# Optimization experiments

Hardware: AMD Instinct MI355X
Metric: run time of the kernel (lower is better)

## Reference

```python
import jax, jax.numpy as jnp
import numpy as np

EPS = 1e-5  # torch InstanceNorm2d default eps


def _attend(x_q, x_kv, Wq, Wk, Wv, Wo):
    # x_q, x_kv: [B, N, C]
    B, N, _ = x_q.shape
    q = x_q @ Wq            # [B, N, CH]
    k = x_kv @ Wk           # [B, N, CH]
    v = x_kv @ Wv           # [B, N, CH]
    CH = q.shape[-1]
    # rearrange 'b n c -> n (b c)' : [N, B*CH]; the torch repeat across batch
    # is redundant (same K/V for every query sample), so we keep one copy.
    kcat = jnp.transpose(k, (1, 0, 2)).reshape(N, B * CH)
    vcat = jnp.transpose(v, (1, 0, 2)).reshape(N, B * CH)
    # scores[b, i, j] = sum_n q[b, n, i] * kcat[n, j]  -> [B, CH, B*CH]
    scores = jnp.einsum('bni,nj->bij', q, kcat)
    # InstanceNorm2d(1): per-sample normalization over the (CH, B*CH) plane
    mu = scores.mean(axis=(1, 2), keepdims=True)
    var = scores.var(axis=(1, 2), keepdims=True)  # biased var, matches torch
    scores = (scores - mu) * jax.lax.rsqrt(var + EPS)
    attn = jax.nn.softmax(scores, axis=-1)        # softmax over j (dim=3)
    # ctx[b, n, i] = sum_j attn[b, i, j] * vcat[n, j]  -> [B, N, CH]
    ctx = jnp.einsum('bij,nj->bni', attn, vcat)
    return ctx @ Wo  # [B, N, C]


def setup_inputs() -> dict:
    key = jax.random.key(0)
    k0, k1, k2, k3, k4 = jax.random.split(key, 5)
    C, H = 64, 8
    CH = C * H
    emb = jax.random.normal(k0, (16, 2048, C), dtype=jnp.float32)
    s = 0.02
    Wq = jax.random.normal(k1, (C, CH), dtype=jnp.float32) * s
    Wk = jax.random.normal(k2, (C, CH), dtype=jnp.float32) * s
    Wv = jax.random.normal(k3, (C, CH), dtype=jnp.float32) * s
    Wo = jax.random.normal(k4, (CH, C), dtype=jnp.float32) * s
    return {"emb": emb, "Wq": Wq, "Wk": Wk, "Wv": Wv, "Wo": Wo}


def reference(emb, Wq, Wk, Wv, Wo):
    emb_l, emb_u = jnp.split(emb, 2, axis=0)
    emb_u_sg = jax.lax.stop_gradient(emb_u)  # emb_u is detached in the torch code
    out_u2l = _attend(emb_u_sg, emb_l, Wq, Wk, Wv, Wo)
    out_l2u = _attend(emb_l, emb_u_sg, Wq, Wk, Wv, Wo)
    return jnp.concatenate([out_l2u, out_u2l], axis=0)
```

## Files before the change

kernel.cpp:

```cpp
#include <hip/hip_runtime.h>
#include <hip/hip_fp16.h>

#define EPS 1e-5f

typedef __attribute__((ext_vector_type(8))) _Float16 half8;
typedef __attribute__((ext_vector_type(4))) _Float16 half4;
typedef __attribute__((ext_vector_type(4))) float float4v;

__device__ __forceinline__ float rv_from(const float* sums2, int db)
{
    float s1 = 0.f, s2 = 0.f;
#pragma unroll
    for (int p = 0; p < 8; p++) {
        s1 += sums2[(db * 8 + p) * 2];
        s2 += sums2[(db * 8 + p) * 2 + 1];
    }
    const float inv = 1.f / 2097152.f;
    float mu = s1 * inv;
    float var = s2 * inv - mu * mu;
    return rsqrtf(var + EPS);
}

__global__ __launch_bounds__(256)
void convT_k(const float* __restrict__ emb, const float* __restrict__ Wq,
             const float* __restrict__ Wk, const float* __restrict__ Wv,
             const float* __restrict__ Wo, __half* __restrict__ emb16,
             __half* __restrict__ embT16, __half* __restrict__ WkT16,
             __half* __restrict__ Wo16, __half* __restrict__ Wv16,
             float* __restrict__ GWQpart, float* __restrict__ wsp,
             __half* __restrict__ WqT16h, __half* __restrict__ WqT16l)
{
    __shared__ __align__(16) char smem[18432];
    const int tid = threadIdx.x;
    const int bid = blockIdx.x;

    if (bid < 256) {
        __half (*T)[136] = (__half(*)[136])smem;
        const int bb = bid >> 4;
        const int t0 = (bid & 15) * 128;
        const float* src = emb + (long long)bb * 131072 + (long long)t0 * 64;
        __half* d16 = emb16 + (long long)bb * 131072 + (long long)t0 * 64;
#pragma unroll
        for (int it = 0; it < 8; it++) {
            int e = (tid + it * 256) * 4;
            int t = e >> 6, c = e & 63;
            float4 v = *(const float4*)(src + t * 64 + c);
            half4 h;
            h[0] = (_Float16)v.x; h[1] = (_Float16)v.y;
            h[2] = (_Float16)v.z; h[3] = (_Float16)v.w;
            *(half4*)(d16 + t * 64 + c) = h;
            T[c + 0][t] = (__half)h[0];
            T[c + 1][t] = (__half)h[1];
            T[c + 2][t] = (__half)h[2];
            T[c + 3][t] = (__half)h[3];
        }
        __syncthreads();
        __half* dT = embT16 + (long long)bb * 131072 + t0;
#pragma unroll
        for (int it = 0; it < 4; it++) {
            int e = (tid + it * 256) * 8;
            int c = e >> 7, tt = e & 127;
            *(half8*)(dT + (long long)c * 2048 + tt) = *(const half8*)&T[c][tt];
        }
    } else if (bid < 272) {
        float (*t)[65] = (float(*)[65])smem;
        const int which = (bid - 256) >> 3;
        const int c0 = ((bid - 256) & 7) * 64;
        const int c = tid & 63, r4 = tid >> 6;
        if (which == 0) {
#pragma unroll
            for (int rr = r4; rr < 64; rr += 4)
                t[rr][c] = Wk[rr * 512 + c0 + c];
            __syncthreads();
#pragma unroll
            for (int rr = r4; rr < 64; rr += 4)
                WkT16[(c0 + rr) * 64 + c] = __float2half(t[c][rr]);
        } else {
#pragma unroll
            for (int rr = r4; rr < 64; rr += 4)
                t[rr][c] = Wo[(c0 + rr) * 64 + c];
            __syncthreads();
#pragma unroll
            for (int rr = r4; rr < 64; rr += 4)
                Wo16[rr * 512 + c0 + c] = __float2half(t[c][rr]);
        }
    } else if (bid < 280) {
        const int base = (bid - 272) * 4096;
#pragma unroll
        for (int it = 0; it < 4; it++) {
            int e = base + (tid + it * 256) * 4;
            float4 v = *(const float4*)(Wv + e);
            *(__half2*)(Wv16 + e)     = __floats2half2_rn(v.x, v.y);
            *(__half2*)(Wv16 + e + 2) = __floats2half2_rn(v.z, v.w);
        }
    } else if (bid < 296) {
        float (*Wl)[68] = (float(*)[68])smem;
        const int t2 = bid - 280;
        const int which = t2 >> 3;
        const int sl = t2 & 7;
        const int i0 = sl * 64;
        const float* W = which ? Wq : Wk;
        float* Gout = GWQpart + (long long)(which * 8 + sl) * 4096;
#pragma unroll
        for (int it = 0; it < 4; it++) {
            int e = tid + it * 256;
            int cc = e >> 4, i4 = (e & 15) * 4;
            *(float4*)&Wl[cc][i4] = *(const float4*)(W + cc * 512 + i0 + i4);
        }
        __syncthreads();
        if (tid < 64) {
            float s = 0.f;
#pragma unroll
            for (int j = 0; j < 64; j++) s += Wl[tid][j];
            wsp[(which * 8 + sl) * 64 + tid] = s;
        }
        const int cr = tid >> 2, cg = (tid & 3) * 16;
        float p[16] = {};
        for (int k = 0; k < 64; k++) {
            float a = Wl[cr][k];
#pragma unroll
            for (int j = 0; j < 16; j++) p[j] += a * Wl[cg + j][k];
        }
#pragma unroll
        for (int j = 0; j < 16; j++)
            Gout[cr * 64 + cg + j] = p[j];
    } else {
        float (*t)[65] = (float(*)[65])smem;
        const int i0 = (bid - 296) * 64;
        const int c = tid & 63, r4 = tid >> 6;
#pragma unroll
        for (int rr = r4; rr < 64; rr += 4)
            t[rr][c] = Wq[rr * 512 + i0 + c];
        __syncthreads();
#pragma unroll
        for (int rr = r4; rr < 64; rr += 4) {
            float x = t[c][rr];
            __half h = __float2half(x);
            WqT16h[(i0 + rr) * 64 + c] = h;
            WqT16l[(i0 + rr) * 64 + c] = __float2half(x - __half2float(h));
        }
    }
}

__global__ __launch_bounds__(256)
void gram_k(const __half* __restrict__ embT16, float* __restrict__ Gpart)
{
    const int tid = threadIdx.x, bid = blockIdx.x;
    const int ks = bid >> 6, z6 = bid & 63;
    const int b = z6 >> 3, bp = z6 & 7;
    const int lane = tid & 63, w = tid >> 6, q = lane >> 4, l16 = lane & 15;

    const __half* Arow = embT16 + (long long)b * 131072 +
                         (long long)(w * 16 + l16) * 2048 + ks * 256 + q * 8;
    const __half* Bbase = embT16 + 1048576 + (long long)bp * 131072 +
                          (long long)l16 * 2048 + ks * 256 + q * 8;

    float4v acc[4];
#pragma unroll
    for (int nt = 0; nt < 4; nt++) acc[nt] = (float4v)0.f;

#pragma unroll
    for (int t0 = 0; t0 < 256; t0 += 32) {
        half8 af = *(const half8*)(Arow + t0);
        half8 bf[4];
#pragma unroll
        for (int nt = 0; nt < 4; nt++)
            bf[nt] = *(const half8*)(Bbase + nt * 32768 + t0);
#pragma unroll
        for (int nt = 0; nt < 4; nt++)
            acc[nt] = __builtin_amdgcn_mfma_f32_16x16x32_f16(af, bf[nt], acc[nt], 0, 0, 0);
    }

    float* Gz = Gpart + (long long)ks * 262144 + (long long)z6 * 4096;
#pragma unroll
    for (int nt = 0; nt < 4; nt++)
#pragma unroll
        for (int t = 0; t < 4; t++) {
            int m = w * 16 + q * 4 + t;
            Gz[m * 64 + nt * 16 + l16] = acc[nt][t];
        }
}

__global__ __launch_bounds__(256)
void stats2_k(const float* __restrict__ Gpart, const float* __restrict__ GWQpart,
              const float* __restrict__ wsp, __half* __restrict__ GT16h,
              __half* __restrict__ GT16l, float* __restrict__ sums2)
{
    __shared__ float Graw[64][68], Gs[64][68], GQs[64][68], GWs[64][68];
    __shared__ float wqsS[64], wksS[64];
    const int tid = threadIdx.x;
    const int z = blockIdx.x;
    const int d = z >> 6, b = (z >> 3) & 7, bp = z & 7;
    const int zm = d ? (bp * 8 + b) : (b * 8 + bp);

    for (int f = tid * 4; f < 4096; f += 1024) {
        float4 g = make_float4(0.f, 0.f, 0.f, 0.f);
        float4 gw = g, gq = g;
#pragma unroll
        for (int s = 0; s < 8; s++) {
            float4 p = *(const float4*)(Gpart + (long long)s * 262144 + (long long)zm * 4096 + f);
            g.x += p.x; g.y += p.y; g.z += p.z; g.w += p.w;
            float4 w1 = *(const float4*)(GWQpart + (long long)s * 4096 + f);
            gw.x += w1.x; gw.y += w1.y; gw.z += w1.z; gw.w += w1.w;
            float4 q1 = *(const float4*)(GWQpart + (long long)(8 + s) * 4096 + f);
            gq.x += q1.x; gq.y += q1.y; gq.z += q1.z; gq.w += q1.w;
        }
        int rr = f >> 6, cc = f & 63;
        *(float4*)&Graw[rr][cc] = g;
        *(float4*)&GWs[rr][cc] = gw;
        *(float4*)&GQs[rr][cc] = gq;
    }
    if (tid < 64) {
        float a = 0.f, bsum = 0.f;
#pragma unroll
        for (int s = 0; s < 8; s++) {
            bsum += wsp[s * 64 + tid];
            a    += wsp[(8 + s) * 64 + tid];
        }
        wqsS[tid] = a; wksS[tid] = bsum;
    }
    __syncthreads();
    for (int e = tid; e < 4096; e += 256) {
        int rr = e >> 6, cc = e & 63;
        Gs[rr][cc] = d ? Graw[cc][rr] : Graw[rr][cc];
    }
    __syncthreads();
    for (int e = tid; e < 4096; e += 256) {
        int cp = e >> 6, c = e & 63;
        float g = Gs[c][cp];
        __half h = __float2half(g);
        GT16h[(long long)z * 4096 + e] = h;
        GT16l[(long long)z * 4096 + e] = __float2half(g - __half2float(h));
    }

    const int r = tid >> 2;
    const int c0 = (tid & 3) * 16;
    float p1[16] = {}, p2[16] = {};
    for (int k = 0; k < 64; k++) {
        float gq = GQs[r][k], g = Gs[r][k];
#pragma unroll
        for (int j = 0; j < 16; j++) {
            p1[j] += gq * Gs[k][c0 + j];
            p2[j] += g  * GWs[k][c0 + j];
        }
    }
    float s2 = 0.f;
#pragma unroll
    for (int j = 0; j < 16; j++) s2 += p1[j] * p2[j];
    float s1 = 0.f;
    const float wq = wqsS[r];
#pragma unroll
    for (int j = 0; j < 16; j++) s1 += wq * Gs[r][c0 + j] * wksS[c0 + j];

    const int lane = tid & 63, w = tid >> 6;
#pragma unroll
    for (int off = 32; off; off >>= 1) {
        s1 += __shfl_down(s1, off, 64);
        s2 += __shfl_down(s2, off, 64);
    }
    __shared__ float r1[4], r2[4];
    if (lane == 0) { r1[w] = s1; r2[w] = s2; }
    __syncthreads();
    if (tid == 0) {
        sums2[z * 2]     = r1[0] + r1[1] + r1[2] + r1[3];
        sums2[z * 2 + 1] = r2[0] + r2[1] + r2[2] + r2[3];
    }
}

__global__ __launch_bounds__(256)
void mfma_ms(const __half* __restrict__ WqT16h, const __half* __restrict__ WqT16l,
             const __half* __restrict__ GT16h, const __half* __restrict__ GT16l,
             const __half* __restrict__ WkT16, const __half* __restrict__ Wv16,
             const float* __restrict__ sums2, float* __restrict__ rsp,
             __half* __restrict__ Mt)
{
    __shared__ __half Es[128][72];
    __shared__ __half Wks[2][64][72];
    __shared__ __half Wvs[2][64][72];
    __shared__ __half Pt[128][72];

    const int tid = threadIdx.x;
    const int z = blockIdx.x;
    const int it = blockIdx.y;
    const int db = z >> 3, bp = z & 7;
    const int i0base = it * 128;

    const int lane = tid & 63, w = tid >> 6, q = lane >> 4, l16 = lane & 15;
    const float rv = rv_from(sums2, db);
    const int srow = tid >> 2, sc8 = (tid & 3) * 16;

    half8 gk0 = *(const half8*)(WkT16 + (long long)srow * 64 + sc8);
    half8 gk1 = *(const half8*)(WkT16 + (long long)srow * 64 + sc8 + 8);
    half8 gv0 = *(const half8*)(Wv16 + (long long)srow * 512 + sc8);
    half8 gv1 = *(const half8*)(Wv16 + (long long)srow * 512 + sc8 + 8);

    {
        const __half* Wh = WqT16h + (long long)i0base * 64;
        const __half* Wl = WqT16l + (long long)i0base * 64;
        const __half* Gh = GT16h + (long long)z * 4096;
        const __half* Gl = GT16l + (long long)z * 4096;
        float4v eacc[2][4];
#pragma unroll
        for (int a = 0; a < 2; a++)
#pragma unroll
            for (int b2 = 0; b2 < 4; b2++) eacc[a][b2] = (float4v)0.f;
#pragma unroll
        for (int kc = 0; kc < 64; kc += 32) {
            half8 ah[2], al[2], bh[4], bl[4];
#pragma unroll
            for (int mt = 0; mt < 2; mt++) {
                const int i = w * 32 + mt * 16 + l16;
                ah[mt] = *(const half8*)(Wh + i * 64 + kc + q * 8);
                al[mt] = *(const half8*)(Wl + i * 64 + kc + q * 8);
            }
#pragma unroll
            for (int nt = 0; nt < 4; nt++) {
                const int cp = nt * 16 + l16;
                bh[nt] = *(const half8*)(Gh + cp * 64 + kc + q * 8);
                bl[nt] = *(const half8*)(Gl + cp * 64 + kc + q * 8);
            }
#pragma unroll
            for (int mt = 0; mt < 2; mt++)
#pragma unroll
                for (int nt = 0; nt < 4; nt++) {
                    eacc[mt][nt] = __builtin_amdgcn_mfma_f32_16x16x32_f16(ah[mt], bh[nt], eacc[mt][nt], 0, 0, 0);
                    eacc[mt][nt] = __builtin_amdgcn_mfma_f32_16x16x32_f16(ah[mt], bl[nt], eacc[mt][nt], 0, 0, 0);
                    eacc[mt][nt] = __builtin_amdgcn_mfma_f32_16x16x32_f16(al[mt], bh[nt], eacc[mt][nt], 0, 0, 0);
                }
        }
#pragma unroll
        for (int mt = 0; mt < 2; mt++)
#pragma unroll
            for (int nt = 0; nt < 4; nt++)
#pragma unroll
                for (int t = 0; t < 4; t++)
                    Es[w * 32 + mt * 16 + q * 4 + t][nt * 16 + l16] =
                        __float2half(eacc[mt][nt][t]);
    }
    *(half8*)&Wks[0][srow][sc8]     = gk0;
    *(half8*)&Wks[0][srow][sc8 + 8] = gk1;
    *(half8*)&Wvs[0][srow][sc8]     = gv0;
    *(half8*)&Wvs[0][srow][sc8 + 8] = gv1;
    __syncthreads();

    float4v macc[2][4];
#pragma unroll
    for (int a = 0; a < 2; a++)
#pragma unroll
        for (int b2 = 0; b2 < 4; b2++) macc[a][b2] = (float4v)0.f;
    float rsacc[2] = {0.f, 0.f};

    int cur = 0;
    for (int c = 0; c < 8; c++) {
        const int ch0 = c * 64;
        if (c < 7) {
            const int chn = ch0 + 64;
            gk0 = *(const half8*)(WkT16 + (long long)(chn + srow) * 64 + sc8);
            gk1 = *(const half8*)(WkT16 + (long long)(chn + srow) * 64 + sc8 + 8);
            gv0 = *(const half8*)(Wv16 + (long long)srow * 512 + chn + sc8);
            gv1 = *(const half8*)(Wv16 + (long long)srow * 512 + chn + sc8 + 8);
        }

        float4v sacc[4][2];
#pragma unroll
        for (int a = 0; a < 4; a++)
#pragma unroll
            for (int b2 = 0; b2 < 2; b2++) sacc[a][b2] = (float4v)0.f;
#pragma unroll
        for (int kc = 0; kc < 64; kc += 32) {
            half8 af[4], bf[2];
#pragma unroll
            for (int mt = 0; mt < 4; mt++)
                af[mt] = *(const half8*)&Wks[cur][mt * 16 + l16][kc + q * 8];
#pragma unroll
            for (int nt = 0; nt < 2; nt++)
                bf[nt] = *(const half8*)&Es[w * 32 + nt * 16 + l16][kc + q * 8];
#pragma unroll
            for (int mt = 0; mt < 4; mt++)
#pragma unroll
                for (int nt = 0; nt < 2; nt++)
                    sacc[mt][nt] = __builtin_amdgcn_mfma_f32_16x16x32_f16(af[mt], bf[nt], sacc[mt][nt], 0, 0, 0);
        }

#pragma unroll
        for (int nt = 0; nt < 2; nt++) {
            const int i = w * 32 + nt * 16 + l16;
#pragma unroll
            for (int mt = 0; mt < 4; mt++) {
                float e0 = __expf(rv * sacc[mt][nt][0]);
                float e1 = __expf(rv * sacc[mt][nt][1]);
                float e2 = __expf(rv * sacc[mt][nt][2]);
                float e3 = __expf(rv * sacc[mt][nt][3]);
                rsacc[nt] += e0 + e1 + e2 + e3;
                const int ch = mt * 16 + q * 4;
                *(__half2*)&Pt[i][ch]     = __floats2half2_rn(e0, e1);
                *(__half2*)&Pt[i][ch + 2] = __floats2half2_rn(e2, e3);
            }
        }

#pragma unroll
        for (int kc = 0; kc < 64; kc += 32) {
            half8 af2[2], bf2[4];
#pragma unroll
            for (int mt2 = 0; mt2 < 2; mt2++)
                af2[mt2] = *(const half8*)&Pt[w * 32 + mt2 * 16 + l16][kc + q * 8];
#pragma unroll
            for (int nt2 = 0; nt2 < 4; nt2++)
                bf2[nt2] = *(const half8*)&Wvs[cur][nt2 * 16 + l16][kc + q * 8];
#pragma unroll
            for (int mt2 = 0; mt2 < 2; mt2++)
#pragma unroll
                for (int nt2 = 0; nt2 < 4; nt2++)
                    macc[mt2][nt2] = __builtin_amdgcn_mfma_f32_16x16x32_f16(af2[mt2], bf2[nt2], macc[mt2][nt2], 0, 0, 0);
        }

        if (c < 7) {
            *(half8*)&Wks[cur ^ 1][srow][sc8]     = gk0;
            *(half8*)&Wks[cur ^ 1][srow][sc8 + 8] = gk1;
            *(half8*)&Wvs[cur ^ 1][srow][sc8]     = gv0;
            *(half8*)&Wvs[cur ^ 1][srow][sc8 + 8] = gv1;
        }
        __syncthreads();
        cur ^= 1;
    }

#pragma unroll
    for (int nt = 0; nt < 2; nt++) {
        float p = rsacc[nt];
        p += __shfl_xor(p, 16, 64);
        p += __shfl_xor(p, 32, 64);
        if (q == 0)
            rsp[(long long)(db * 512 + i0base + w * 32 + nt * 16 + l16) * 8 + bp] = p;
    }

    __half (*MtS)[144] = (__half(*)[144])&Pt[0][0];
    const float sc = 1.f / 4096.f;
#pragma unroll
    for (int mt2 = 0; mt2 < 2; mt2++)
#pragma unroll
        for (int nt2 = 0; nt2 < 4; nt2++) {
            const int cp = nt2 * 16 + l16;
            const int il = w * 32 + mt2 * 16 + q * 4;
#pragma unroll
            for (int t = 0; t < 4; t++)
                MtS[cp][il + t] = __float2half(macc[mt2][nt2][t] * sc);
        }
    __syncthreads();
    __half* Mz = Mt + (long long)z * 32768;
    {
        const int row = tid >> 2, seg = (tid & 3) * 32;
#pragma unroll
        for (int j = 0; j < 4; j++)
            *(half8*)(Mz + (long long)row * 512 + i0base + seg + j * 8) =
                *(const half8*)&MtS[row][seg + j * 8];
    }
}

__global__ __launch_bounds__(256)
void mfma_n(const __half* __restrict__ Mt, const __half* __restrict__ Wo16,
            const float* __restrict__ rsp, __half* __restrict__ NT)
{
    __shared__ __half Mts[64][72];
    __shared__ __half Wos[64][72];
    __shared__ float invrS[64];
    const int tid = threadIdx.x;
    const int db = blockIdx.x >> 3, bp = blockIdx.x & 7;
    const __half* Mz = Mt + (long long)(db * 8 + bp) * 32768;
    const int lane = tid & 63, w = tid >> 6, q = lane >> 4, l16 = lane & 15;

    float4v acc[4];
#pragma unroll
    for (int mt = 0; mt < 4; mt++) acc[mt] = (float4v)0.f;

    const int srow = tid >> 2, sc8 = (tid & 3) * 16;

    for (int i0 = 0; i0 < 512; i0 += 64) {
        __syncthreads();
        if (tid < 64) {
            const float* rp = rsp + (long long)(db * 512 + i0 + tid) * 8;
            float4 a = *(const float4*)rp;
            float4 b = *(const float4*)(rp + 4);
            invrS[tid] = 4096.0f / (a.x + a.y + a.z + a.w + b.x + b.y + b.z + b.w);
        }
        __syncthreads();
#pragma unroll
        for (int h = 0; h < 2; h++) {
            half8 v = *(const half8*)(Mz + (long long)srow * 512 + i0 + sc8 + h * 8);
            half8 o;
#pragma unroll
            for (int j = 0; j < 8; j++)
                o[j] = (_Float16)((float)v[j] * invrS[sc8 + h * 8 + j]);
            *(half8*)&Mts[srow][sc8 + h * 8] = o;
            *(half8*)&Wos[srow][sc8 + h * 8] =
                *(const half8*)(Wo16 + (long long)srow * 512 + i0 + sc8 + h * 8);
        }
        __syncthreads();
#pragma unroll
        for (int kc = 0; kc < 64; kc += 32) {
            half8 af[4];
#pragma unroll
            for (int mt = 0; mt < 4; mt++)
                af[mt] = *(const half8*)&Mts[mt * 16 + l16][kc + q * 8];
            half8 bf = *(const half8*)&Wos[w * 16 + l16][kc + q * 8];
#pragma unroll
            for (int mt = 0; mt < 4; mt++)
                acc[mt] = __builtin_amdgcn_mfma_f32_16x16x32_f16(af[mt], bf, acc[mt], 0, 0, 0);
        }
    }

    __half* Nz = NT + (long long)db * 32768;
    const int o = w * 16 + l16;
#pragma unroll
    for (int mt = 0; mt < 4; mt++) {
        const int k = bp * 64 + mt * 16 + q * 4;
        *(__half2*)(Nz + (long long)o * 512 + k)     = __floats2half2_rn(acc[mt][0], acc[mt][1]);
        *(__half2*)(Nz + (long long)o * 512 + k + 2) = __floats2half2_rn(acc[mt][2], acc[mt][3]);
    }
}

__global__ __launch_bounds__(256)
void mfma_out(const __half* __restrict__ emb16, const __half* __restrict__ NT,
              float* __restrict__ out)
{
    const int tid = threadIdx.x;
    const int db = blockIdx.y;
    const int d = db >> 3;
    const int n0 = blockIdx.x * 128;
    const __half* Xb = emb16 + (long long)(1 - d) * 1048576;
    const __half* Bz = NT + (long long)db * 32768;

    const int lane = tid & 63, w = tid >> 6, q = lane >> 4, l16 = lane & 15;

    float4v acc[2][4];
#pragma unroll
    for (int a = 0; a < 2; a++)
#pragma unroll
        for (int b = 0; b < 4; b++) acc[a][b] = (float4v)0.f;

    for (int bp = 0; bp < 8; bp++) {
        const __half* src = Xb + (long long)bp * 131072 + (long long)n0 * 64;
#pragma unroll
        for (int kc = 0; kc < 64; kc += 32) {
            half8 af[2], bf[4];
#pragma unroll
            for (int mt = 0; mt < 2; mt++)
                af[mt] = *(const half8*)(src + (long long)(w * 32 + mt * 16 + l16) * 64 + kc + q * 8);
#pragma unroll
            for (int ot = 0; ot < 4; ot++)
                bf[ot] = *(const half8*)(Bz + (long long)(ot * 16 + l16) * 512 + bp * 64 + kc + q * 8);
#pragma unroll
            for (int mt = 0; mt < 2; mt++)
#pragma unroll
                for (int ot = 0; ot < 4; ot++)
                    acc[mt][ot] = __builtin_amdgcn_mfma_f32_16x16x32_f16(af[mt], bf[ot], acc[mt][ot], 0, 0, 0);
        }
    }

    float* Od = out + (long long)db * 131072;
#pragma unroll
    for (int mt = 0; mt < 2; mt++)
#pragma unroll
        for (int ot = 0; ot < 4; ot++)
#pragma unroll
            for (int t = 0; t < 4; t++) {
                int n = n0 + w * 32 + mt * 16 + q * 4 + t;
                Od[(long long)n * 64 + ot * 16 + l16] = acc[mt][ot][t];
            }
}

extern "C" void kernel_launch(void* const* d_in, const int* in_sizes, int n_in,
                              void* d_out, int out_size, void* d_ws, size_t ws_size,
                              hipStream_t stream)
{
    const float* emb = (const float*)d_in[0];
    const float* Wq  = (const float*)d_in[1];
    const float* Wk  = (const float*)d_in[2];
    const float* Wv  = (const float*)d_in[3];
    const float* Wo  = (const float*)d_in[4];
    float* out = (float*)d_out;
    float* ws  = (float*)d_ws;

    float* Gpart   = ws;
    float* GWQpart = ws + 2097152;
    float* wsp     = ws + 2162688;
    float* sums2   = ws + 2163712;
    __half* GT16h  = (__half*)(ws + 2163968);
    __half* GT16l  = (__half*)(ws + 2426112);
    float* rsp     = ws + 2688256;
    __half* WkT16  = (__half*)(ws + 2753792);
    __half* Wv16   = (__half*)(ws + 2770176);
    __half* Wo16   = (__half*)(ws + 2786560);
    __half* WqT16h = (__half*)(ws + 2802944);
    __half* WqT16l = (__half*)(ws + 2819328);
    __half* Mt     = (__half*)(ws + 2835712);
    __half* NT     = (__half*)(ws + 4932864);
    __half* emb16  = (__half*)(ws + 5195008);
    __half* embT16 = (__half*)(ws + 6243584);

    convT_k<<<304, 256, 0, stream>>>(emb, Wq, Wk, Wv, Wo, emb16, embT16,
                                     WkT16, Wo16, Wv16, GWQpart, wsp,
                                     WqT16h, WqT16l);

    gram_k<<<512, 256, 0, stream>>>(embT16, Gpart);

    stats2_k<<<128, 256, 0, stream>>>(Gpart, GWQpart, wsp, GT16h, GT16l, sums2);

    mfma_ms<<<dim3(128, 4), 256, 0, stream>>>(WqT16h, WqT16l, GT16h, GT16l,
                                              WkT16, Wv16, sums2, rsp, Mt);

    mfma_n<<<128, 256, 0, stream>>>(Mt, Wo16, rsp, NT);

    mfma_out<<<dim3(16, 16), 256, 0, stream>>>(emb16, NT, out);
}
```

Before: 156.9 us.

## Fuse all six stages into one persistent kernel with atomic grid barriers

```diff
diff --git a/kernel.cpp b/kernel.cpp
--- a/kernel.cpp
+++ b/kernel.cpp
@@ -21,564 +21,28 @@
     return rsqrtf(var + EPS);
 }
 
-__global__ __launch_bounds__(256)
-void convT_k(const float* __restrict__ emb, const float* __restrict__ Wq,
-             const float* __restrict__ Wk, const float* __restrict__ Wv,
-             const float* __restrict__ Wo, __half* __restrict__ emb16,
-             __half* __restrict__ embT16, __half* __restrict__ WkT16,
-             __half* __restrict__ Wo16, __half* __restrict__ Wv16,
-             float* __restrict__ GWQpart, float* __restrict__ wsp,
-             __half* __restrict__ WqT16h, __half* __restrict__ WqT16l)
+__device__ __forceinline__ void grid_bar(int* ctr, int idx)
 {
-    __shared__ __align__(16) char smem[18432];
+    __syncthreads();
+    if (threadIdx.x == 0) {
+        __threadfence();
+        __hip_atomic_fetch_add(ctr + idx, 1, __ATOMIC_RELEASE, __HIP_MEMORY_SCOPE_AGENT);
+        while (__hip_atomic_load(ctr + idx, __ATOMIC_ACQUIRE, __HIP_MEMORY_SCOPE_AGENT) < 512)
+            __builtin_amdgcn_s_sleep(8);
+        __threadfence();
+    }
+    __syncthreads();
+}
+
+__global__ __launch_bounds__(256, 2)
+void mega_k(const float* __restrict__ emb, const float* __restrict__ Wq,
+            const float* __restrict__ Wk, const float* __restrict__ Wv,
+            const float* __restrict__ Wo, float* __restrict__ ws,
+            float* __restrict__ out)
+{
+    __shared__ __align__(16) char SM[73728];
     const int tid = threadIdx.x;
     const int bid = blockIdx.x;
-
-    if (bid < 256) {
-        __half (*T)[136] = (__half(*)[136])smem;
-        const int bb = bid >> 4;
-        const int t0 = (bid & 15) * 128;
-        const float* src = emb + (long long)bb * 131072 + (long long)t0 * 64;
-        __half* d16 = emb16 + (long long)bb * 131072 + (long long)t0 * 64;
-#pragma unroll
-        for (int it = 0; it < 8; it++) {
-            int e = (tid + it * 256) * 4;
-            int t = e >> 6, c = e & 63;
-            float4 v = *(const float4*)(src + t * 64 + c);
-            half4 h;
-            h[0] = (_Float16)v.x; h[1] = (_Float16)v.y;
-            h[2] = (_Float16)v.z; h[3] = (_Float16)v.w;
-            *(half4*)(d16 + t * 64 + c) = h;
-            T[c + 0][t] = (__half)h[0];
-            T[c + 1][t] = (__half)h[1];
-            T[c + 2][t] = (__half)h[2];
-            T[c + 3][t] = (__half)h[3];
-        }
-        __syncthreads();
-        __half* dT = embT16 + (long long)bb * 131072 + t0;
-#pragma unroll
-        for (int it = 0; it < 4; it++) {
-            int e = (tid + it * 256) * 8;
-            int c = e >> 7, tt = e & 127;
-            *(half8*)(dT + (long long)c * 2048 + tt) = *(const half8*)&T[c][tt];
-        }
-    } else if (bid < 272) {
-        float (*t)[65] = (float(*)[65])smem;
-        const int which = (bid - 256) >> 3;
-        const int c0 = ((bid - 256) & 7) * 64;
-        const int c = tid & 63, r4 = tid >> 6;
-        if (which == 0) {
-#pragma unroll
-            for (int rr = r4; rr < 64; rr += 4)
-                t[rr][c] = Wk[rr * 512 + c0 + c];
-            __syncthreads();
-#pragma unroll
-            for (int rr = r4; rr < 64; rr += 4)
-                WkT16[(c0 + rr) * 64 + c] = __float2half(t[c][rr]);
-        } else {
-#pragma unroll
-            for (int rr = r4; rr < 64; rr += 4)
-                t[rr][c] = Wo[(c0 + rr) * 64 + c];
-            __syncthreads();
-#pragma unroll
-            for (int rr = r4; rr < 64; rr += 4)
-                Wo16[rr * 512 + c0 + c] = __float2half(t[c][rr]);
-        }
-    } else if (bid < 280) {
-        const int base = (bid - 272) * 4096;
-#pragma unroll
-        for (int it = 0; it < 4; it++) {
-            int e = base + (tid + it * 256) * 4;
-            float4 v = *(const float4*)(Wv + e);
-            *(__half2*)(Wv16 + e)     = __floats2half2_rn(v.x, v.y);
-            *(__half2*)(Wv16 + e + 2) = __floats2half2_rn(v.z, v.w);
-        }
-    } else if (bid < 296) {
-        float (*Wl)[68] = (float(*)[68])smem;
-        const int t2 = bid - 280;
-        const int which = t2 >> 3;
-        const int sl = t2 & 7;
-        const int i0 = sl * 64;
-        const float* W = which ? Wq : Wk;
-        float* Gout = GWQpart + (long long)(which * 8 + sl) * 4096;
-#pragma unroll
-        for (int it = 0; it < 4; it++) {
-            int e = tid + it * 256;
-            int cc = e >> 4, i4 = (e & 15) * 4;
-            *(float4*)&Wl[cc][i4] = *(const float4*)(W + cc * 512 + i0 + i4);
-        }
-        __syncthreads();
-        if (tid < 64) {
-            float s = 0.f;
-#pragma unroll
-            for (int j = 0; j < 64; j++) s += Wl[tid][j];
-            wsp[(which * 8 + sl) * 64 + tid] = s;
-        }
-        const int cr = tid >> 2, cg = (tid & 3) * 16;
-        float p[16] = {};
-        for (int k = 0; k < 64; k++) {
-            float a = Wl[cr][k];
-#pragma unroll
-            for (int j = 0; j < 16; j++) p[j] += a * Wl[cg + j][k];
-        }
-#pragma unroll
-        for (int j = 0; j < 16; j++)
-            Gout[cr * 64 + cg + j] = p[j];
-    } else {
-        float (*t)[65] = (float(*)[65])smem;
-        const int i0 = (bid - 296) * 64;
-        const int c = tid & 63, r4 = tid >> 6;
-#pragma unroll
-        for (int rr = r4; rr < 64; rr += 4)
-            t[rr][c] = Wq[rr * 512 + i0 + c];
-        __syncthreads();
-#pragma unroll
-        for (int rr = r4; rr < 64; rr += 4) {
-            float x = t[c][rr];
-            __half h = __float2half(x);
-            WqT16h[(i0 + rr) * 64 + c] = h;
-            WqT16l[(i0 + rr) * 64 + c] = __float2half(x - __half2float(h));
-        }
-    }
-}
-
-__global__ __launch_bounds__(256)
-void gram_k(const __half* __restrict__ embT16, float* __restrict__ Gpart)
-{
-    const int tid = threadIdx.x, bid = blockIdx.x;
-    const int ks = bid >> 6, z6 = bid & 63;
-    const int b = z6 >> 3, bp = z6 & 7;
-    const int lane = tid & 63, w = tid >> 6, q = lane >> 4, l16 = lane & 15;
-
-    const __half* Arow = embT16 + (long long)b * 131072 +
-                         (long long)(w * 16 + l16) * 2048 + ks * 256 + q * 8;
-    const __half* Bbase = embT16 + 1048576 + (long long)bp * 131072 +
-                          (long long)l16 * 2048 + ks * 256 + q * 8;
-
-    float4v acc[4];
-#pragma unroll
-    for (int nt = 0; nt < 4; nt++) acc[nt] = (float4v)0.f;
-
-#pragma unroll
-    for (int t0 = 0; t0 < 256; t0 += 32) {
-        half8 af = *(const half8*)(Arow + t0);
-        half8 bf[4];
-#pragma unroll
-        for (int nt = 0; nt < 4; nt++)
-            bf[nt] = *(const half8*)(Bbase + nt * 32768 + t0);
-#pragma unroll
-        for (int nt = 0; nt < 4; nt++)
-            acc[nt] = __builtin_amdgcn_mfma_f32_16x16x32_f16(af, bf[nt], acc[nt], 0, 0, 0);
-    }
-
-    float* Gz = Gpart + (long long)ks * 262144 + (long long)z6 * 4096;
-#pragma unroll
-    for (int nt = 0; nt < 4; nt++)
-#pragma unroll
-        for (int t = 0; t < 4; t++) {
-            int m = w * 16 + q * 4 + t;
-            Gz[m * 64 + nt * 16 + l16] = acc[nt][t];
-        }
-}
-
-__global__ __launch_bounds__(256)
-void stats2_k(const float* __restrict__ Gpart, const float* __restrict__ GWQpart,
-              const float* __restrict__ wsp, __half* __restrict__ GT16h,
-              __half* __restrict__ GT16l, float* __restrict__ sums2)
-{
-    __shared__ float Graw[64][68], Gs[64][68], GQs[64][68], GWs[64][68];
-    __shared__ float wqsS[64], wksS[64];
-    const int tid = threadIdx.x;
-    const int z = blockIdx.x;
-    const int d = z >> 6, b = (z >> 3) & 7, bp = z & 7;
-    const int zm = d ? (bp * 8 + b) : (b * 8 + bp);
-
-    for (int f = tid * 4; f < 4096; f += 1024) {
-        float4 g = make_float4(0.f, 0.f, 0.f, 0.f);
-        float4 gw = g, gq = g;
-#pragma unroll
-        for (int s = 0; s < 8; s++) {
-            float4 p = *(const float4*)(Gpart + (long long)s * 262144 + (long long)zm * 4096 + f);
-            g.x += p.x; g.y += p.y; g.z += p.z; g.w += p.w;
-            float4 w1 = *(const float4*)(GWQpart + (long long)s * 4096 + f);
-            gw.x += w1.x; gw.y += w1.y; gw.z += w1.z; gw.w += w1.w;
-            float4 q1 = *(const float4*)(GWQpart + (long long)(8 + s) * 4096 + f);
-            gq.x += q1.x; gq.y += q1.y; gq.z += q1.z; gq.w += q1.w;
-        }
-        int rr = f >> 6, cc = f & 63;
-        *(float4*)&Graw[rr][cc] = g;
-        *(float4*)&GWs[rr][cc] = gw;
-        *(float4*)&GQs[rr][cc] = gq;
-    }
-    if (tid < 64) {
-        float a = 0.f, bsum = 0.f;
-#pragma unroll
-        for (int s = 0; s < 8; s++) {
-            bsum += wsp[s * 64 + tid];
-            a    += wsp[(8 + s) * 64 + tid];
-        }
-        wqsS[tid] = a; wksS[tid] = bsum;
-    }
-    __syncthreads();
-    for (int e = tid; e < 4096; e += 256) {
-        int rr = e >> 6, cc = e & 63;
-        Gs[rr][cc] = d ? Graw[cc][rr] : Graw[rr][cc];
-    }
-    __syncthreads();
-    for (int e = tid; e < 4096; e += 256) {
-        int cp = e >> 6, c = e & 63;
-        float g = Gs[c][cp];
-        __half h = __float2half(g);
-        GT16h[(long long)z * 4096 + e] = h;
-        GT16l[(long long)z * 4096 + e] = __float2half(g - __half2float(h));
-    }
-
-    const int r = tid >> 2;
-    const int c0 = (tid & 3) * 16;
-    float p1[16] = {}, p2[16] = {};
-    for (int k = 0; k < 64; k++) {
-        float gq = GQs[r][k], g = Gs[r][k];
-#pragma unroll
-        for (int j = 0; j < 16; j++) {
-            p1[j] += gq * Gs[k][c0 + j];
-            p2[j] += g  * GWs[k][c0 + j];
-        }
-    }
-    float s2 = 0.f;
-#pragma unroll
-    for (int j = 0; j < 16; j++) s2 += p1[j] * p2[j];
-    float s1 = 0.f;
-    const float wq = wqsS[r];
-#pragma unroll
-    for (int j = 0; j < 16; j++) s1 += wq * Gs[r][c0 + j] * wksS[c0 + j];
-
-    const int lane = tid & 63, w = tid >> 6;
-#pragma unroll
-    for (int off = 32; off; off >>= 1) {
-        s1 += __shfl_down(s1, off, 64);
-        s2 += __shfl_down(s2, off, 64);
-    }
-    __shared__ float r1[4], r2[4];
-    if (lane == 0) { r1[w] = s1; r2[w] = s2; }
-    __syncthreads();
-    if (tid == 0) {
-        sums2[z * 2]     = r1[0] + r1[1] + r1[2] + r1[3];
-        sums2[z * 2 + 1] = r2[0] + r2[1] + r2[2] + r2[3];
-    }
-}
-
-__global__ __launch_bounds__(256)
-void mfma_ms(const __half* __restrict__ WqT16h, const __half* __restrict__ WqT16l,
-             const __half* __restrict__ GT16h, const __half* __restrict__ GT16l,
-             const __half* __restrict__ WkT16, const __half* __restrict__ Wv16,
-             const float* __restrict__ sums2, float* __restrict__ rsp,
-             __half* __restrict__ Mt)
-{
-    __shared__ __half Es[128][72];
-    __shared__ __half Wks[2][64][72];
-    __shared__ __half Wvs[2][64][72];
-    __shared__ __half Pt[128][72];
-
-    const int tid = threadIdx.x;
-    const int z = blockIdx.x;
-    const int it = blockIdx.y;
-    const int db = z >> 3, bp = z & 7;
-    const int i0base = it * 128;
-
-    const int lane = tid & 63, w = tid >> 6, q = lane >> 4, l16 = lane & 15;
-    const float rv = rv_from(sums2, db);
-    const int srow = tid >> 2, sc8 = (tid & 3) * 16;
-
-    half8 gk0 = *(const half8*)(WkT16 + (long long)srow * 64 + sc8);
-    half8 gk1 = *(const half8*)(WkT16 + (long long)srow * 64 + sc8 + 8);
-    half8 gv0 = *(const half8*)(Wv16 + (long long)srow * 512 + sc8);
-    half8 gv1 = *(const half8*)(Wv16 + (long long)srow * 512 + sc8 + 8);
-
-    {
-        const __half* Wh = WqT16h + (long long)i0base * 64;
-        const __half* Wl = WqT16l + (long long)i0base * 64;
-        const __half* Gh = GT16h + (long long)z * 4096;
-        const __half* Gl = GT16l + (long long)z * 4096;
-        float4v eacc[2][4];
-#pragma unroll
-        for (int a = 0; a < 2; a++)
-#pragma unroll
-            for (int b2 = 0; b2 < 4; b2++) eacc[a][b2] = (float4v)0.f;
-#pragma unroll
-        for (int kc = 0; kc < 64; kc += 32) {
-            half8 ah[2], al[2], bh[4], bl[4];
-#pragma unroll
-            for (int mt = 0; mt < 2; mt++) {
-                const int i = w * 32 + mt * 16 + l16;
-                ah[mt] = *(const half8*)(Wh + i * 64 + kc + q * 8);
-                al[mt] = *(const half8*)(Wl + i * 64 + kc + q * 8);
-            }
-#pragma unroll
-            for (int nt = 0; nt < 4; nt++) {
-                const int cp = nt * 16 + l16;
-                bh[nt] = *(const half8*)(Gh + cp * 64 + kc + q * 8);
-                bl[nt] = *(const half8*)(Gl + cp * 64 + kc + q * 8);
-            }
-#pragma unroll
-            for (int mt = 0; mt < 2; mt++)
-#pragma unroll
-                for (int nt = 0; nt < 4; nt++) {
-                    eacc[mt][nt] = __builtin_amdgcn_mfma_f32_16x16x32_f16(ah[mt], bh[nt], eacc[mt][nt], 0, 0, 0);
-                    eacc[mt][nt] = __builtin_amdgcn_mfma_f32_16x16x32_f16(ah[mt], bl[nt], eacc[mt][nt], 0, 0, 0);
-                    eacc[mt][nt] = __builtin_amdgcn_mfma_f32_16x16x32_f16(al[mt], bh[nt], eacc[mt][nt], 0, 0, 0);
-                }
-        }
-#pragma unroll
-        for (int mt = 0; mt < 2; mt++)
-#pragma unroll
-            for (int nt = 0; nt < 4; nt++)
-#pragma unroll
-                for (int t = 0; t < 4; t++)
-                    Es[w * 32 + mt * 16 + q * 4 + t][nt * 16 + l16] =
-                        __float2half(eacc[mt][nt][t]);
-    }
-    *(half8*)&Wks[0][srow][sc8]     = gk0;
-    *(half8*)&Wks[0][srow][sc8 + 8] = gk1;
-    *(half8*)&Wvs[0][srow][sc8]     = gv0;
-    *(half8*)&Wvs[0][srow][sc8 + 8] = gv1;
-    __syncthreads();
-
-    float4v macc[2][4];
-#pragma unroll
-    for (int a = 0; a < 2; a++)
-#pragma unroll
-        for (int b2 = 0; b2 < 4; b2++) macc[a][b2] = (float4v)0.f;
-    float rsacc[2] = {0.f, 0.f};
-
-    int cur = 0;
-    for (int c = 0; c < 8; c++) {
-        const int ch0 = c * 64;
-        if (c < 7) {
-            const int chn = ch0 + 64;
-            gk0 = *(const half8*)(WkT16 + (long long)(chn + srow) * 64 + sc8);
-            gk1 = *(const half8*)(WkT16 + (long long)(chn + srow) * 64 + sc8 + 8);
-            gv0 = *(const half8*)(Wv16 + (long long)srow * 512 + chn + sc8);
-            gv1 = *(const half8*)(Wv16 + (long long)srow * 512 + chn + sc8 + 8);
-        }
-
-        float4v sacc[4][2];
-#pragma unroll
-        for (int a = 0; a < 4; a++)
-#pragma unroll
-            for (int b2 = 0; b2 < 2; b2++) sacc[a][b2] = (float4v)0.f;
-#pragma unroll
-        for (int kc = 0; kc < 64; kc += 32) {
-            half8 af[4], bf[2];
-#pragma unroll
-            for (int mt = 0; mt < 4; mt++)
-                af[mt] = *(const half8*)&Wks[cur][mt * 16 + l16][kc + q * 8];
-#pragma unroll
-            for (int nt = 0; nt < 2; nt++)
-                bf[nt] = *(const half8*)&Es[w * 32 + nt * 16 + l16][kc + q * 8];
-#pragma unroll
-            for (int mt = 0; mt < 4; mt++)
-#pragma unroll
-                for (int nt = 0; nt < 2; nt++)
-                    sacc[mt][nt] = __builtin_amdgcn_mfma_f32_16x16x32_f16(af[mt], bf[nt], sacc[mt][nt], 0, 0, 0);
-        }
-
-#pragma unroll
-        for (int nt = 0; nt < 2; nt++) {
-            const int i = w * 32 + nt * 16 + l16;
-#pragma unroll
-            for (int mt = 0; mt < 4; mt++) {
-                float e0 = __expf(rv * sacc[mt][nt][0]);
-                float e1 = __expf(rv * sacc[mt][nt][1]);
-                float e2 = __expf(rv * sacc[mt][nt][2]);
-                float e3 = __expf(rv * sacc[mt][nt][3]);
-                rsacc[nt] += e0 + e1 + e2 + e3;
-                const int ch = mt * 16 + q * 4;
-                *(__half2*)&Pt[i][ch]     = __floats2half2_rn(e0, e1);
-                *(__half2*)&Pt[i][ch + 2] = __floats2half2_rn(e2, e3);
-            }
-        }
-
-#pragma unroll
-        for (int kc = 0; kc < 64; kc += 32) {
-            half8 af2[2], bf2[4];
-#pragma unroll
-            for (int mt2 = 0; mt2 < 2; mt2++)
-                af2[mt2] = *(const half8*)&Pt[w * 32 + mt2 * 16 + l16][kc + q * 8];
-#pragma unroll
-            for (int nt2 = 0; nt2 < 4; nt2++)
-                bf2[nt2] = *(const half8*)&Wvs[cur][nt2 * 16 + l16][kc + q * 8];
-#pragma unroll
-            for (int mt2 = 0; mt2 < 2; mt2++)
-#pragma unroll
-                for (int nt2 = 0; nt2 < 4; nt2++)
-                    macc[mt2][nt2] = __builtin_amdgcn_mfma_f32_16x16x32_f16(af2[mt2], bf2[nt2], macc[mt2][nt2], 0, 0, 0);
-        }
-
-        if (c < 7) {
-            *(half8*)&Wks[cur ^ 1][srow][sc8]     = gk0;
-            *(half8*)&Wks[cur ^ 1][srow][sc8 + 8] = gk1;
-            *(half8*)&Wvs[cur ^ 1][srow][sc8]     = gv0;
-            *(half8*)&Wvs[cur ^ 1][srow][sc8 + 8] = gv1;
-        }
-        __syncthreads();
-        cur ^= 1;
-    }
-
-#pragma unroll
-    for (int nt = 0; nt < 2; nt++) {
-        float p = rsacc[nt];
-        p += __shfl_xor(p, 16, 64);
-        p += __shfl_xor(p, 32, 64);
-        if (q == 0)
-            rsp[(long long)(db * 512 + i0base + w * 32 + nt * 16 + l16) * 8 + bp] = p;
-    }
-
-    __half (*MtS)[144] = (__half(*)[144])&Pt[0][0];
-    const float sc = 1.f / 4096.f;
-#pragma unroll
-    for (int mt2 = 0; mt2 < 2; mt2++)
-#pragma unroll
-        for (int nt2 = 0; nt2 < 4; nt2++) {
-            const int cp = nt2 * 16 + l16;
-            const int il = w * 32 + mt2 * 16 + q * 4;
-#pragma unroll
-            for (int t = 0; t < 4; t++)
-                MtS[cp][il + t] = __float2half(macc[mt2][nt2][t] * sc);
-        }
-    __syncthreads();
-    __half* Mz = Mt + (long long)z * 32768;
-    {
-        const int row = tid >> 2, seg = (tid & 3) * 32;
-#pragma unroll
-        for (int j = 0; j < 4; j++)
-            *(half8*)(Mz + (long long)row * 512 + i0base + seg + j * 8) =
-                *(const half8*)&MtS[row][seg + j * 8];
-    }
-}
-
-__global__ __launch_bounds__(256)
-void mfma_n(const __half* __restrict__ Mt, const __half* __restrict__ Wo16,
-            const float* __restrict__ rsp, __half* __restrict__ NT)
-{
-    __shared__ __half Mts[64][72];
-    __shared__ __half Wos[64][72];
-    __shared__ float invrS[64];
-    const int tid = threadIdx.x;
-    const int db = blockIdx.x >> 3, bp = blockIdx.x & 7;
-    const __half* Mz = Mt + (long long)(db * 8 + bp) * 32768;
-    const int lane = tid & 63, w = tid >> 6, q = lane >> 4, l16 = lane & 15;
-
-    float4v acc[4];
-#pragma unroll
-    for (int mt = 0; mt < 4; mt++) acc[mt] = (float4v)0.f;
-
-    const int srow = tid >> 2, sc8 = (tid & 3) * 16;
-
-    for (int i0 = 0; i0 < 512; i0 += 64) {
-        __syncthreads();
-        if (tid < 64) {
-            const float* rp = rsp + (long long)(db * 512 + i0 + tid) * 8;
-            float4 a = *(const float4*)rp;
-            float4 b = *(const float4*)(rp + 4);
-            invrS[tid] = 4096.0f / (a.x + a.y + a.z + a.w + b.x + b.y + b.z + b.w);
-        }
-        __syncthreads();
-#pragma unroll
-        for (int h = 0; h < 2; h++) {
-            half8 v = *(const half8*)(Mz + (long long)srow * 512 + i0 + sc8 + h * 8);
-            half8 o;
-#pragma unroll
-            for (int j = 0; j < 8; j++)
-                o[j] = (_Float16)((float)v[j] * invrS[sc8 + h * 8 + j]);
-            *(half8*)&Mts[srow][sc8 + h * 8] = o;
-            *(half8*)&Wos[srow][sc8 + h * 8] =
-                *(const half8*)(Wo16 + (long long)srow * 512 + i0 + sc8 + h * 8);
-        }
-        __syncthreads();
-#pragma unroll
-        for (int kc = 0; kc < 64; kc += 32) {
-            half8 af[4];
-#pragma unroll
-            for (int mt = 0; mt < 4; mt++)
-                af[mt] = *(const half8*)&Mts[mt * 16 + l16][kc + q * 8];
-            half8 bf = *(const half8*)&Wos[w * 16 + l16][kc + q * 8];
-#pragma unroll
-            for (int mt = 0; mt < 4; mt++)
-                acc[mt] = __builtin_amdgcn_mfma_f32_16x16x32_f16(af[mt], bf, acc[mt], 0, 0, 0);
-        }
-    }
-
-    __half* Nz = NT + (long long)db * 32768;
-    const int o = w * 16 + l16;
-#pragma unroll
-    for (int mt = 0; mt < 4; mt++) {
-        const int k = bp * 64 + mt * 16 + q * 4;
-        *(__half2*)(Nz + (long long)o * 512 + k)     = __floats2half2_rn(acc[mt][0], acc[mt][1]);
-        *(__half2*)(Nz + (long long)o * 512 + k + 2) = __floats2half2_rn(acc[mt][2], acc[mt][3]);
-    }
-}
-
-__global__ __launch_bounds__(256)
-void mfma_out(const __half* __restrict__ emb16, const __half* __restrict__ NT,
-              float* __restrict__ out)
-{
-    const int tid = threadIdx.x;
-    const int db = blockIdx.y;
-    const int d = db >> 3;
-    const int n0 = blockIdx.x * 128;
-    const __half* Xb = emb16 + (long long)(1 - d) * 1048576;
-    const __half* Bz = NT + (long long)db * 32768;
-
-    const int lane = tid & 63, w = tid >> 6, q = lane >> 4, l16 = lane & 15;
-
-    float4v acc[2][4];
-#pragma unroll
-    for (int a = 0; a < 2; a++)
-#pragma unroll
-        for (int b = 0; b < 4; b++) acc[a][b] = (float4v)0.f;
-
-    for (int bp = 0; bp < 8; bp++) {
-        const __half* src = Xb + (long long)bp * 131072 + (long long)n0 * 64;
-#pragma unroll
-        for (int kc = 0; kc < 64; kc += 32) {
-            half8 af[2], bf[4];
-#pragma unroll
-            for (int mt = 0; mt < 2; mt++)
-                af[mt] = *(const half8*)(src + (long long)(w * 32 + mt * 16 + l16) * 64 + kc + q * 8);
-#pragma unroll
-            for (int ot = 0; ot < 4; ot++)
-                bf[ot] = *(const half8*)(Bz + (long long)(ot * 16 + l16) * 512 + bp * 64 + kc + q * 8);
-#pragma unroll
-            for (int mt = 0; mt < 2; mt++)
-#pragma unroll
-                for (int ot = 0; ot < 4; ot++)
-                    acc[mt][ot] = __builtin_amdgcn_mfma_f32_16x16x32_f16(af[mt], bf[ot], acc[mt][ot], 0, 0, 0);
-        }
-    }
-
-    float* Od = out + (long long)db * 131072;
-#pragma unroll
-    for (int mt = 0; mt < 2; mt++)
-#pragma unroll
-        for (int ot = 0; ot < 4; ot++)
-#pragma unroll
-            for (int t = 0; t < 4; t++) {
-                int n = n0 + w * 32 + mt * 16 + q * 4 + t;
-                Od[(long long)n * 64 + ot * 16 + l16] = acc[mt][ot][t];
-            }
-}
-
-extern "C" void kernel_launch(void* const* d_in, const int* in_sizes, int n_in,
-                              void* d_out, int out_size, void* d_ws, size_t ws_size,
-                              hipStream_t stream)
-{
-    const float* emb = (const float*)d_in[0];
-    const float* Wq  = (const float*)d_in[1];
-    const float* Wk  = (const float*)d_in[2];
-    const float* Wv  = (const float*)d_in[3];
-    const float* Wo  = (const float*)d_in[4];
-    float* out = (float*)d_out;
-    float* ws  = (float*)d_ws;
 
     float* Gpart   = ws;
     float* GWQpart = ws + 2097152;
@@ -596,19 +60,546 @@
     __half* NT     = (__half*)(ws + 4932864);
     __half* emb16  = (__half*)(ws + 5195008);
     __half* embT16 = (__half*)(ws + 6243584);
-
-    convT_k<<<304, 256, 0, stream>>>(emb, Wq, Wk, Wv, Wo, emb16, embT16,
-                                     WkT16, Wo16, Wv16, GWQpart, wsp,
-                                     WqT16h, WqT16l);
-
-    gram_k<<<512, 256, 0, stream>>>(embT16, Gpart);
-
-    stats2_k<<<128, 256, 0, stream>>>(Gpart, GWQpart, wsp, GT16h, GT16l, sums2);
-
-    mfma_ms<<<dim3(128, 4), 256, 0, stream>>>(WqT16h, WqT16l, GT16h, GT16l,
-                                              WkT16, Wv16, sums2, rsp, Mt);
-
-    mfma_n<<<128, 256, 0, stream>>>(Mt, Wo16, rsp, NT);
-
-    mfma_out<<<dim3(16, 16), 256, 0, stream>>>(emb16, NT, out);
+    int* ctr       = (int*)(ws + 7292160);
+
+    if (bid < 304) {
+        if (bid < 256) {
+            __half (*T)[136] = (__half(*)[136])SM;
+            const int bb = bid >> 4;
+            const int t0 = (bid & 15) * 128;
+            const float* src = emb + (long long)bb * 131072 + (long long)t0 * 64;
+            __half* d16 = emb16 + (long long)bb * 131072 + (long long)t0 * 64;
+#pragma unroll
+            for (int it = 0; it < 8; it++) {
+                int e = (tid + it * 256) * 4;
+                int t = e >> 6, c = e & 63;
+                float4 v = *(const float4*)(src + t * 64 + c);
+                half4 h;
+                h[0] = (_Float16)v.x; h[1] = (_Float16)v.y;
+                h[2] = (_Float16)v.z; h[3] = (_Float16)v.w;
+                *(half4*)(d16 + t * 64 + c) = h;
+                T[c + 0][t] = (__half)h[0];
+                T[c + 1][t] = (__half)h[1];
+                T[c + 2][t] = (__half)h[2];
+                T[c + 3][t] = (__half)h[3];
+            }
+            __syncthreads();
+            __half* dT = embT16 + (long long)bb * 131072 + t0;
+#pragma unroll
+            for (int it = 0; it < 4; it++) {
+                int e = (tid + it * 256) * 8;
+                int c = e >> 7, tt = e & 127;
+                *(half8*)(dT + (long long)c * 2048 + tt) = *(const half8*)&T[c][tt];
+            }
+        } else if (bid < 272) {
+            float (*t)[65] = (float(*)[65])SM;
+            const int which = (bid - 256) >> 3;
+            const int c0 = ((bid - 256) & 7) * 64;
+            const int c = tid & 63, r4 = tid >> 6;
+            if (which == 0) {
+#pragma unroll
+                for (int rr = r4; rr < 64; rr += 4)
+                    t[rr][c] = Wk[rr * 512 + c0 + c];
+                __syncthreads();
+#pragma unroll
+                for (int rr = r4; rr < 64; rr += 4)
+                    WkT16[(c0 + rr) * 64 + c] = __float2half(t[c][rr]);
+            } else {
+#pragma unroll
+                for (int rr = r4; rr < 64; rr += 4)
+                    t[rr][c] = Wo[(c0 + rr) * 64 + c];
+                __syncthreads();
+#pragma unroll
+                for (int rr = r4; rr < 64; rr += 4)
+                    Wo16[rr * 512 + c0 + c] = __float2half(t[c][rr]);
+            }
+        } else if (bid < 280) {
+            const int base = (bid - 272) * 4096;
+#pragma unroll
+            for (int it = 0; it < 4; it++) {
+                int e = base + (tid + it * 256) * 4;
+                float4 v = *(const float4*)(Wv + e);
+                *(__half2*)(Wv16 + e)     = __floats2half2_rn(v.x, v.y);
+                *(__half2*)(Wv16 + e + 2) = __floats2half2_rn(v.z, v.w);
+            }
+        } else if (bid < 296) {
+            float (*Wl)[68] = (float(*)[68])SM;
+            const int t2 = bid - 280;
+            const int which = t2 >> 3;
+            const int sl = t2 & 7;
+            const int i0 = sl * 64;
+            const float* W = which ? Wq : Wk;
+            float* Gout = GWQpart + (long long)(which * 8 + sl) * 4096;
+#pragma unroll
+            for (int it = 0; it < 4; it++) {
+                int e = tid + it * 256;
+                int cc = e >> 4, i4 = (e & 15) * 4;
+                *(float4*)&Wl[cc][i4] = *(const float4*)(W + cc * 512 + i0 + i4);
+            }
+            __syncthreads();
+            if (tid < 64) {
+                float s = 0.f;
+#pragma unroll
+                for (int j = 0; j < 64; j++) s += Wl[tid][j];
+                wsp[(which * 8 + sl) * 64 + tid] = s;
+            }
+            const int cr = tid >> 2, cg = (tid & 3) * 16;
+            float p[16] = {};
+            for (int k = 0; k < 64; k++) {
+                float a = Wl[cr][k];
+#pragma unroll
+                for (int j = 0; j < 16; j++) p[j] += a * Wl[cg + j][k];
+            }
+#pragma unroll
+            for (int j = 0; j < 16; j++)
+                Gout[cr * 64 + cg + j] = p[j];
+        } else {
+            float (*t)[65] = (float(*)[65])SM;
+            const int i0 = (bid - 296) * 64;
+            const int c = tid & 63, r4 = tid >> 6;
+#pragma unroll
+            for (int rr = r4; rr < 64; rr += 4)
+                t[rr][c] = Wq[rr * 512 + i0 + c];
+            __syncthreads();
+#pragma unroll
+            for (int rr = r4; rr < 64; rr += 4) {
+                float x = t[c][rr];
+                __half h = __float2half(x);
+                WqT16h[(i0 + rr) * 64 + c] = h;
+                WqT16l[(i0 + rr) * 64 + c] = __float2half(x - __half2float(h));
+            }
+        }
+    }
+    grid_bar(ctr, 0);
+
+    {
+        const int ks = bid >> 6, z6 = bid & 63;
+        const int b = z6 >> 3, bp = z6 & 7;
+        const int lane = tid & 63, w = tid >> 6, q = lane >> 4, l16 = lane & 15;
+
+        const __half* Arow = embT16 + (long long)b * 131072 +
+                             (long long)(w * 16 + l16) * 2048 + ks * 256 + q * 8;
+        const __half* Bbase = embT16 + 1048576 + (long long)bp * 131072 +
+                              (long long)l16 * 2048 + ks * 256 + q * 8;
+
+        float4v acc[4];
+#pragma unroll
+        for (int nt = 0; nt < 4; nt++) acc[nt] = (float4v)0.f;
+
+#pragma unroll
+        for (int t0 = 0; t0 < 256; t0 += 32) {
+            half8 af = *(const half8*)(Arow + t0);
+            half8 bf[4];
+#pragma unroll
+            for (int nt = 0; nt < 4; nt++)
+                bf[nt] = *(const half8*)(Bbase + nt * 32768 + t0);
+#pragma unroll
+            for (int nt = 0; nt < 4; nt++)
+                acc[nt] = __builtin_amdgcn_mfma_f32_16x16x32_f16(af, bf[nt], acc[nt], 0, 0, 0);
+        }
+
+        float* Gz = Gpart + (long long)ks * 262144 + (long long)z6 * 4096;
+#pragma unroll
+        for (int nt = 0; nt < 4; nt++)
+#pragma unroll
+            for (int t = 0; t < 4; t++) {
+                int m = w * 16 + q * 4 + t;
+                Gz[m * 64 + nt * 16 + l16] = acc[nt][t];
+            }
+    }
+    grid_bar(ctr, 1);
+
+    if (bid < 128) {
+        float (*Graw)[68] = (float(*)[68])SM;
+        float (*Gs)[68]   = (float(*)[68])(SM + 17408);
+        float (*GQs)[68]  = (float(*)[68])(SM + 34816);
+        float (*GWs)[68]  = (float(*)[68])(SM + 52224);
+        float* wqsS = (float*)(SM + 69632);
+        float* wksS = (float*)(SM + 69888);
+        float* r1   = (float*)(SM + 70144);
+        float* r2   = (float*)(SM + 70160);
+
+        const int z = bid;
+        const int d = z >> 6, b = (z >> 3) & 7, bp = z & 7;
+        const int zm = d ? (bp * 8 + b) : (b * 8 + bp);
+
+        for (int f = tid * 4; f < 4096; f += 1024) {
+            float4 g = make_float4(0.f, 0.f, 0.f, 0.f);
+            float4 gw = g, gq = g;
+#pragma unroll
+            for (int s = 0; s < 8; s++) {
+                float4 p = *(const float4*)(Gpart + (long long)s * 262144 + (long long)zm * 4096 + f);
+                g.x += p.x; g.y += p.y; g.z += p.z; g.w += p.w;
+                float4 w1 = *(const float4*)(GWQpart + (long long)s * 4096 + f);
+                gw.x += w1.x; gw.y += w1.y; gw.z += w1.z; gw.w += w1.w;
+                float4 q1 = *(const float4*)(GWQpart + (long long)(8 + s) * 4096 + f);
+                gq.x += q1.x; gq.y += q1.y; gq.z += q1.z; gq.w += q1.w;
+            }
+            int rr = f >> 6, cc = f & 63;
+            *(float4*)&Graw[rr][cc] = g;
+            *(float4*)&GWs[rr][cc] = gw;
+            *(float4*)&GQs[rr][cc] = gq;
+        }
+        if (tid < 64) {
+            float a = 0.f, bsum = 0.f;
+#pragma unroll
+            for (int s = 0; s < 8; s++) {
+                bsum += wsp[s * 64 + tid];
+                a    += wsp[(8 + s) * 64 + tid];
+            }
+            wqsS[tid] = a; wksS[tid] = bsum;
+        }
+        __syncthreads();
+        for (int e = tid; e < 4096; e += 256) {
+            int rr = e >> 6, cc = e & 63;
+            Gs[rr][cc] = d ? Graw[cc][rr] : Graw[rr][cc];
+        }
+        __syncthreads();
+        for (int e = tid; e < 4096; e += 256) {
+            int cp = e >> 6, c = e & 63;
+            float g = Gs[c][cp];
+            __half h = __float2half(g);
+            GT16h[(long long)z * 4096 + e] = h;
+            GT16l[(long long)z * 4096 + e] = __float2half(g - __half2float(h));
+        }
+
+        const int r = tid >> 2;
+        const int c0 = (tid & 3) * 16;
+        float p1[16] = {}, p2[16] = {};
+        for (int k = 0; k < 64; k++) {
+            float gq = GQs[r][k], g = Gs[r][k];
+#pragma unroll
+            for (int j = 0; j < 16; j++) {
+                p1[j] += gq * Gs[k][c0 + j];
+                p2[j] += g  * GWs[k][c0 + j];
+            }
+        }
+        float s2 = 0.f;
+#pragma unroll
+        for (int j = 0; j < 16; j++) s2 += p1[j] * p2[j];
+        float s1 = 0.f;
+        const float wq = wqsS[r];
+#pragma unroll
+        for (int j = 0; j < 16; j++) s1 += wq * Gs[r][c0 + j] * wksS[c0 + j];
+
+        const int lane = tid & 63, w = tid >> 6;
+#pragma unroll
+        for (int off = 32; off; off >>= 1) {
+            s1 += __shfl_down(s1, off, 64);
+            s2 += __shfl_down(s2, off, 64);
+        }
+        if (lane == 0) { r1[w] = s1; r2[w] = s2; }
+        __syncthreads();
+        if (tid == 0) {
+            sums2[z * 2]     = r1[0] + r1[1] + r1[2] + r1[3];
+            sums2[z * 2 + 1] = r2[0] + r2[1] + r2[2] + r2[3];
+        }
+    }
+    grid_bar(ctr, 2);
+
+    {
+        __half (*Es)[72]      = (__half(*)[72])SM;
+        __half (*Wks)[64][72] = (__half(*)[64][72])(SM + 18432);
+        __half (*Wvs)[64][72] = (__half(*)[64][72])(SM + 36864);
+        __half (*Pt)[72]      = (__half(*)[72])(SM + 55296);
+
+        const int z = bid & 127;
+        const int it = bid >> 7;
+        const int db = z >> 3, bp = z & 7;
+        const int i0base = it * 128;
+
+        const int lane = tid & 63, w = tid >> 6, q = lane >> 4, l16 = lane & 15;
+        const float rv = rv_from(sums2, db);
+        const int srow = tid >> 2, sc8 = (tid & 3) * 16;
+
+        half8 gk0 = *(const half8*)(WkT16 + (long long)srow * 64 + sc8);
+        half8 gk1 = *(const half8*)(WkT16 + (long long)srow * 64 + sc8 + 8);
+        half8 gv0 = *(const half8*)(Wv16 + (long long)srow * 512 + sc8);
+        half8 gv1 = *(const half8*)(Wv16 + (long long)srow * 512 + sc8 + 8);
+
+        {
+            const __half* Wh = WqT16h + (long long)i0base * 64;
+            const __half* Wl = WqT16l + (long long)i0base * 64;
+            const __half* Gh = GT16h + (long long)z * 4096;
+            const __half* Gl = GT16l + (long long)z * 4096;
+            float4v eacc[2][4];
+#pragma unroll
+            for (int a = 0; a < 2; a++)
+#pragma unroll
+                for (int b2 = 0; b2 < 4; b2++) eacc[a][b2] = (float4v)0.f;
+#pragma unroll
+            for (int kc = 0; kc < 64; kc += 32) {
+                half8 ah[2], al[2], bh[4], bl[4];
+#pragma unroll
+                for (int mt = 0; mt < 2; mt++) {
+                    const int i = w * 32 + mt * 16 + l16;
+                    ah[mt] = *(const half8*)(Wh + i * 64 + kc + q * 8);
+                    al[mt] = *(const half8*)(Wl + i * 64 + kc + q * 8);
+                }
+#pragma unroll
+                for (int nt = 0; nt < 4; nt++) {
+                    const int cp = nt * 16 + l16;
+                    bh[nt] = *(const half8*)(Gh + cp * 64 + kc + q * 8);
+                    bl[nt] = *(const half8*)(Gl + cp * 64 + kc + q * 8);
+                }
+#pragma unroll
+                for (int mt = 0; mt < 2; mt++)
+#pragma unroll
+                    for (int nt = 0; nt < 4; nt++) {
+                        eacc[mt][nt] = __builtin_amdgcn_mfma_f32_16x16x32_f16(ah[mt], bh[nt], eacc[mt][nt], 0, 0, 0);
+                        eacc[mt][nt] = __builtin_amdgcn_mfma_f32_16x16x32_f16(ah[mt], bl[nt], eacc[mt][nt], 0, 0, 0);
+                        eacc[mt][nt] = __builtin_amdgcn_mfma_f32_16x16x32_f16(al[mt], bh[nt], eacc[mt][nt], 0, 0, 0);
+                    }
+            }
+#pragma unroll
+            for (int mt = 0; mt < 2; mt++)
+#pragma unroll
+                for (int nt = 0; nt < 4; nt++)
+#pragma unroll
+                    for (int t = 0; t < 4; t++)
+                        Es[w * 32 + mt * 16 + q * 4 + t][nt * 16 + l16] =
+                            __float2half(eacc[mt][nt][t]);
+        }
+        *(half8*)&Wks[0][srow][sc8]     = gk0;
+        *(half8*)&Wks[0][srow][sc8 + 8] = gk1;
+        *(half8*)&Wvs[0][srow][sc8]     = gv0;
+        *(half8*)&Wvs[0][srow][sc8 + 8] = gv1;
+        __syncthreads();
+
+        float4v macc[2][4];
+#pragma unroll
+        for (int a = 0; a < 2; a++)
+#pragma unroll
+            for (int b2 = 0; b2 < 4; b2++) macc[a][b2] = (float4v)0.f;
+        float rsacc[2] = {0.f, 0.f};
+
+        int cur = 0;
+        for (int c = 0; c < 8; c++) {
+            const int ch0 = c * 64;
+            if (c < 7) {
+                const int chn = ch0 + 64;
+                gk0 = *(const half8*)(WkT16 + (long long)(chn + srow) * 64 + sc8);
+                gk1 = *(const half8*)(WkT16 + (long long)(chn + srow) * 64 + sc8 + 8);
+                gv0 = *(const half8*)(Wv16 + (long long)srow * 512 + chn + sc8);
+                gv1 = *(const half8*)(Wv16 + (long long)srow * 512 + chn + sc8 + 8);
+            }
+
+            float4v sacc[4][2];
+#pragma unroll
+            for (int a = 0; a < 4; a++)
+#pragma unroll
+                for (int b2 = 0; b2 < 2; b2++) sacc[a][b2] = (float4v)0.f;
+#pragma unroll
+            for (int kc = 0; kc < 64; kc += 32) {
+                half8 af[4], bf[2];
+#pragma unroll
+                for (int mt = 0; mt < 4; mt++)
+                    af[mt] = *(const half8*)&Wks[cur][mt * 16 + l16][kc + q * 8];
+#pragma unroll
+                for (int nt = 0; nt < 2; nt++)
+                    bf[nt] = *(const half8*)&Es[w * 32 + nt * 16 + l16][kc + q * 8];
+#pragma unroll
+                for (int mt = 0; mt < 4; mt++)
+#pragma unroll
+                    for (int nt = 0; nt < 2; nt++)
+                        sacc[mt][nt] = __builtin_amdgcn_mfma_f32_16x16x32_f16(af[mt], bf[nt], sacc[mt][nt], 0, 0, 0);
+            }
+
+#pragma unroll
+            for (int nt = 0; nt < 2; nt++) {
+                const int i = w * 32 + nt * 16 + l16;
+#pragma unroll
+                for (int mt = 0; mt < 4; mt++) {
+                    float e0 = __expf(rv * sacc[mt][nt][0]);
+                    float e1 = __expf(rv * sacc[mt][nt][1]);
+                    float e2 = __expf(rv * sacc[mt][nt][2]);
+                    float e3 = __expf(rv * sacc[mt][nt][3]);
+                    rsacc[nt] += e0 + e1 + e2 + e3;
+                    const int ch = mt * 16 + q * 4;
+                    *(__half2*)&Pt[i][ch]     = __floats2half2_rn(e0, e1);
+                    *(__half2*)&Pt[i][ch + 2] = __floats2half2_rn(e2, e3);
+                }
+            }
+
+#pragma unroll
+            for (int kc = 0; kc < 64; kc += 32) {
+                half8 af2[2], bf2[4];
+#pragma unroll
+                for (int mt2 = 0; mt2 < 2; mt2++)
+                    af2[mt2] = *(const half8*)&Pt[w * 32 + mt2 * 16 + l16][kc + q * 8];
+#pragma unroll
+                for (int nt2 = 0; nt2 < 4; nt2++)
+                    bf2[nt2] = *(const half8*)&Wvs[cur][nt2 * 16 + l16][kc + q * 8];
+#pragma unroll
+                for (int mt2 = 0; mt2 < 2; mt2++)
+#pragma unroll
+                    for (int nt2 = 0; nt2 < 4; nt2++)
+                        macc[mt2][nt2] = __builtin_amdgcn_mfma_f32_16x16x32_f16(af2[mt2], bf2[nt2], macc[mt2][nt2], 0, 0, 0);
+            }
+
+            if (c < 7) {
+                *(half8*)&Wks[cur ^ 1][srow][sc8]     = gk0;
+                *(half8*)&Wks[cur ^ 1][srow][sc8 + 8] = gk1;
+                *(half8*)&Wvs[cur ^ 1][srow][sc8]     = gv0;
+                *(half8*)&Wvs[cur ^ 1][srow][sc8 + 8] = gv1;
+            }
+            __syncthreads();
+            cur ^= 1;
+        }
+
+#pragma unroll
+        for (int nt = 0; nt < 2; nt++) {
+            float p = rsacc[nt];
+            p += __shfl_xor(p, 16, 64);
+            p += __shfl_xor(p, 32, 64);
+            if (q == 0)
+                rsp[(long long)(db * 512 + i0base + w * 32 + nt * 16 + l16) * 8 + bp] = p;
+        }
+
+        __half (*MtS)[144] = (__half(*)[144])(SM + 55296);
+        const float sc = 1.f / 4096.f;
+#pragma unroll
+        for (int mt2 = 0; mt2 < 2; mt2++)
+#pragma unroll
+            for (int nt2 = 0; nt2 < 4; nt2++) {
+                const int cp = nt2 * 16 + l16;
+                const int il = w * 32 + mt2 * 16 + q * 4;
+#pragma unroll
+                for (int t = 0; t < 4; t++)
+                    MtS[cp][il + t] = __float2half(macc[mt2][nt2][t] * sc);
+            }
+        __syncthreads();
+        __half* Mz = Mt + (long long)z * 32768;
+        {
+            const int row = tid >> 2, seg = (tid & 3) * 32;
+#pragma unroll
+            for (int j = 0; j < 4; j++)
+                *(half8*)(Mz + (long long)row * 512 + i0base + seg + j * 8) =
+                    *(const half8*)&MtS[row][seg + j * 8];
+        }
+    }
+    grid_bar(ctr, 3);
+
+    if (bid < 128) {
+        __half (*Mts)[72] = (__half(*)[72])SM;
+        __half (*Wos)[72] = (__half(*)[72])(SM + 9216);
+        float* invrS = (float*)(SM + 18432);
+
+        const int db = bid >> 3, bp = bid & 7;
+        const __half* Mz = Mt + (long long)(db * 8 + bp) * 32768;
+        const int lane = tid & 63, w = tid >> 6, q = lane >> 4, l16 = lane & 15;
+
+        float4v acc[4];
+#pragma unroll
+        for (int mt = 0; mt < 4; mt++) acc[mt] = (float4v)0.f;
+
+        const int srow = tid >> 2, sc8 = (tid & 3) * 16;
+
+        for (int i0 = 0; i0 < 512; i0 += 64) {
+            __syncthreads();
+            if (tid < 64) {
+                const float* rp = rsp + (long long)(db * 512 + i0 + tid) * 8;
+                float4 a = *(const float4*)rp;
+                float4 b = *(const float4*)(rp + 4);
+                invrS[tid] = 4096.0f / (a.x + a.y + a.z + a.w + b.x + b.y + b.z + b.w);
+            }
+            __syncthreads();
+#pragma unroll
+            for (int h = 0; h < 2; h++) {
+                half8 v = *(const half8*)(Mz + (long long)srow * 512 + i0 + sc8 + h * 8);
+                half8 o;
+#pragma unroll
+                for (int j = 0; j < 8; j++)
+                    o[j] = (_Float16)((float)v[j] * invrS[sc8 + h * 8 + j]);
+                *(half8*)&Mts[srow][sc8 + h * 8] = o;
+                *(half8*)&Wos[srow][sc8 + h * 8] =
+                    *(const half8*)(Wo16 + (long long)srow * 512 + i0 + sc8 + h * 8);
+            }
+            __syncthreads();
+#pragma unroll
+            for (int kc = 0; kc < 64; kc += 32) {
+                half8 af[4];
+#pragma unroll
+                for (int mt = 0; mt < 4; mt++)
+                    af[mt] = *(const half8*)&Mts[mt * 16 + l16][kc + q * 8];
+                half8 bf = *(const half8*)&Wos[w * 16 + l16][kc + q * 8];
+#pragma unroll
+                for (int mt = 0; mt < 4; mt++)
+                    acc[mt] = __builtin_amdgcn_mfma_f32_16x16x32_f16(af[mt], bf, acc[mt], 0, 0, 0);
+            }
+        }
+
+        __half* Nz = NT + (long long)db * 32768;
+        const int o = w * 16 + l16;
+#pragma unroll
+        for (int mt = 0; mt < 4; mt++) {
+            const int k = bp * 64 + mt * 16 + q * 4;
+            *(__half2*)(Nz + (long long)o * 512 + k)     = __floats2half2_rn(acc[mt][0], acc[mt][1]);
+            *(__half2*)(Nz + (long long)o * 512 + k + 2) = __floats2half2_rn(acc[mt][2], acc[mt][3]);
+        }
+    }
+    grid_bar(ctr, 4);
+
+    if (bid < 256) {
+        const int db = bid >> 4;
+        const int d = db >> 3;
+        const int n0 = (bid & 15) * 128;
+        const __half* Xb = emb16 + (long long)(1 - d) * 1048576;
+        const __half* Bz = NT + (long long)db * 32768;
+
+        const int lane = tid & 63, w = tid >> 6, q = lane >> 4, l16 = lane & 15;
+
+        float4v acc[2][4];
+#pragma unroll
+        for (int a = 0; a < 2; a++)
+#pragma unroll
+            for (int b = 0; b < 4; b++) acc[a][b] = (float4v)0.f;
+
+        for (int bp = 0; bp < 8; bp++) {
+            const __half* src = Xb + (long long)bp * 131072 + (long long)n0 * 64;
+#pragma unroll
+            for (int kc = 0; kc < 64; kc += 32) {
+                half8 af[2], bf[4];
+#pragma unroll
+                for (int mt = 0; mt < 2; mt++)
+                    af[mt] = *(const half8*)(src + (long long)(w * 32 + mt * 16 + l16) * 64 + kc + q * 8);
+#pragma unroll
+                for (int ot = 0; ot < 4; ot++)
+                    bf[ot] = *(const half8*)(Bz + (long long)(ot * 16 + l16) * 512 + bp * 64 + kc + q * 8);
+#pragma unroll
+                for (int mt = 0; mt < 2; mt++)
+#pragma unroll
+                    for (int ot = 0; ot < 4; ot++)
+                        acc[mt][ot] = __builtin_amdgcn_mfma_f32_16x16x32_f16(af[mt], bf[ot], acc[mt][ot], 0, 0, 0);
+            }
+        }
+
+        float* Od = out + (long long)db * 131072;
+#pragma unroll
+        for (int mt = 0; mt < 2; mt++)
+#pragma unroll
+            for (int ot = 0; ot < 4; ot++)
+#pragma unroll
+                for (int t = 0; t < 4; t++) {
+                    int n = n0 + w * 32 + mt * 16 + q * 4 + t;
+                    Od[(long long)n * 64 + ot * 16 + l16] = acc[mt][ot][t];
+                }
+    }
 }
+
+extern "C" void kernel_launch(void* const* d_in, const int* in_sizes, int n_in,
+                              void* d_out, int out_size, void* d_ws, size_t ws_size,
+                              hipStream_t stream)
+{
+    const float* emb = (const float*)d_in[0];
+    const float* Wq  = (const float*)d_in[1];
+    const float* Wk  = (const float*)d_in[2];
+    const float* Wv  = (const float*)d_in[3];
+    const float* Wo  = (const float*)d_in[4];
+    float* out = (float*)d_out;
+    float* ws  = (float*)d_ws;
+
+    hipMemsetAsync((char*)d_ws + 7292160ULL * 4ULL, 0, 32, stream);
+
+    mega_k<<<512, 256, 0, stream>>>(emb, Wq, Wk, Wv, Wo, ws, out);
+}
```

New measurement: 599.1 us. 282% more time.
